# Performance work log

Hardware: AMD Instinct MI355X
Metric: run time of the kernel (lower is better)

The kernel has to match this reference:

```python
import jax, jax.numpy as jnp
import numpy as np

N_MEL = 80; ARNN = 1024; ADIM = 128; EMB = 512; PRE = 256; DRNN = 1024; NF = 32; KS = 31
B = 32; NCTX = 512; T = 500
PAD = (KS - 1) // 2


def setup_inputs() -> dict:
    key = jax.random.key(0)
    ks = jax.random.split(key, 20)
    g = lambda k, shape: jax.random.normal(k, shape, dtype=jnp.float32) * 0.02
    return {
        "memory": jax.random.normal(ks[0], (B, NCTX, EMB), dtype=jnp.float32),
        "decoder_inputs": jax.random.normal(ks[1], (B, N_MEL, T), dtype=jnp.float32),
        "mask": jnp.zeros((B, NCTX), dtype=bool),
        "prenet_w1": g(ks[2], (PRE, N_MEL)),
        "prenet_w2": g(ks[3], (PRE, PRE)),
        "arnn_wih": g(ks[4], (4 * ARNN, PRE + EMB)),
        "arnn_whh": g(ks[5], (4 * ARNN, ARNN)),
        "arnn_bih": jnp.zeros((4 * ARNN,), jnp.float32),
        "arnn_bhh": jnp.zeros((4 * ARNN,), jnp.float32),
        "q_w": g(ks[6], (ADIM, ARNN)),
        "m_w": g(ks[7], (ADIM, EMB)),
        "loc_conv_w": g(ks[8], (NF, 2, KS)),
        "loc_w": g(ks[9], (ADIM, NF)),
        "v_w": g(ks[10], (ADIM,)),
        "drnn_wih": g(ks[11], (4 * DRNN, ARNN + EMB)),
        "drnn_whh": g(ks[12], (4 * DRNN, DRNN)),
        "drnn_bih": jnp.zeros((4 * DRNN,), jnp.float32),
        "drnn_bhh": jnp.zeros((4 * DRNN,), jnp.float32),
        "proj_w": g(ks[13], (N_MEL, DRNN + EMB)),
        "proj_b": jnp.zeros((N_MEL,), jnp.float32),
        "gate_w": g(ks[14], (1, DRNN + EMB)),
        "gate_b": jnp.zeros((1,), jnp.float32),
    }


def _lstm_cell(x, h, c, wih, whh, bih, bhh):
    # PyTorch LSTMCell gate order: i, f, g, o
    z = x @ wih.T + h @ whh.T + bih + bhh
    i, f, g, o = jnp.split(z, 4, axis=-1)
    c2 = jax.nn.sigmoid(f) * c + jax.nn.sigmoid(i) * jnp.tanh(g)
    h2 = jax.nn.sigmoid(o) * jnp.tanh(c2)
    return h2, c2


def reference(memory, decoder_inputs, mask,
              prenet_w1, prenet_w2,
              arnn_wih, arnn_whh, arnn_bih, arnn_bhh,
              q_w, m_w, loc_conv_w, loc_w, v_w,
              drnn_wih, drnn_whh, drnn_bih, drnn_bhh,
              proj_w, proj_b, gate_w, gate_b):
    b, n_ctx, emb = memory.shape
    n_mel, t_out = decoder_inputs.shape[1], decoder_inputs.shape[2]

    # (time, batch, n_mel) with a leading zero go-frame; PreNet (eval: no dropout)
    x = jnp.transpose(decoder_inputs, (2, 0, 1))
    x = jnp.concatenate([jnp.zeros((1, b, n_mel), x.dtype), x], axis=0)
    h = jax.nn.relu(x @ prenet_w1.T)
    h = jax.nn.relu(h @ prenet_w2.T)  # (T+1, B, PRE)
    inputs = h[:-1]  # T decoder steps

    proc_mem = memory @ m_w.T  # (B, n_ctx, ADIM)

    def step(carry, xin):
        ah, ac, dh, dc, aw, awc, actx = carry
        cell_in = jnp.concatenate([xin, actx], axis=-1)
        ah, ac = _lstm_cell(cell_in, ah, ac, arnn_wih, arnn_whh, arnn_bih, arnn_bhh)
        # location-sensitive attention
        aw_cat = jnp.stack([aw, awc], axis=1)  # (B, 2, n_ctx)
        loc = jax.lax.conv_general_dilated(
            aw_cat, loc_conv_w, window_strides=(1,), padding=[(PAD, PAD)],
            dimension_numbers=("NCH", "OIH", "NCH"))  # (B, NF, n_ctx)
        loc = jnp.transpose(loc, (0, 2, 1)) @ loc_w.T  # (B, n_ctx, ADIM)
        q = (ah @ q_w.T)[:, None, :]  # (B, 1, ADIM)
        e = jnp.tanh(q + proc_mem + loc) @ v_w  # (B, n_ctx)
        e = jnp.where(mask, -1e9, e)
        aw = jax.nn.softmax(e, axis=-1)
        actx = jnp.einsum("bn,bne->be", aw, memory)
        awc = awc + aw
        din = jnp.concatenate([ah, actx], axis=-1)
        dh, dc = _lstm_cell(din, dh, dc, drnn_wih, drnn_whh, drnn_bih, drnn_bhh)
        dhc = jnp.concatenate([dh, actx], axis=-1)
        mel = dhc @ proj_w.T + proj_b  # (B, n_mel)
        gate = dhc @ gate_w.T + gate_b  # (B, 1)
        return (ah, ac, dh, dc, aw, awc, actx), (mel, gate[:, 0])

    z32 = lambda *s: jnp.zeros(s, memory.dtype)
    carry0 = (z32(b, ARNN), z32(b, ARNN), z32(b, DRNN), z32(b, DRNN),
              z32(b, n_ctx), z32(b, n_ctx), z32(b, emb))
    _, (mels, gates) = jax.lax.scan(step, carry0, inputs)
    mel_out = jnp.transpose(mels, (1, 2, 0))   # (B, n_mel, T)
    gate_out = jnp.transpose(gates, (1, 0))    # (B, T)
    return mel_out, gate_out
```

## Files before the change

kernel.cpp:

```cpp
#include <hip/hip_runtime.h>

#define NBLK 256
#define NTHR 512

constexpr int kNMel = 80, kArnn = 1024, kAdim = 128, kEmb = 512, kPre = 256;
constexpr int kNF = 32, kKS = 31, kB = 32, kNctx = 512, kT = 500, kPad = 15;

constexpr int KT_A = 56;
constexpr int KT_D = 80;
constexpr int KT_ALL = KT_A + KT_D;

constexpr int OFF_PREB   = 0;
constexpr int OFF_PROCMB = OFF_PREB + kT * kB * kPre / 2;
constexpr int OFF_QWTB   = OFF_PROCMB + kB * kNctx * kAdim / 2;
constexpr int OFF_LWT    = OFF_QWTB + kAdim * kArnn / 2;
constexpr int OFF_STATE  = OFF_LWT + kAdim * 33;
constexpr int OFF_AHB    = OFF_STATE;
constexpr int OFF_DHB    = OFF_AHB + 2 * kB * kArnn / 2;
constexpr int OFF_DH     = OFF_DHB + 2 * kB * kArnn / 2;
constexpr int OFF_AC     = OFF_DH + 2 * kB * kArnn;
constexpr int OFF_DC     = OFF_AC + kB * kArnn;
constexpr int OFF_ACTX   = OFF_DC + kB * kArnn;
constexpr int OFF_AW     = OFF_ACTX + kB * kEmb;
constexpr int OFF_AWC    = OFF_AW + kB * kNctx;
constexpr int OFF_PAW    = OFF_AWC + kB * kNctx;
constexpr int OFF_NUM    = OFF_PAW + kB * kNctx;
constexpr int OFF_DEN    = OFF_NUM + 2 * kB * kEmb;
constexpr int OFF_END    = OFF_DEN + 2 * kB;
constexpr int STATE_SZ   = OFF_END - OFF_STATE;
constexpr int OFF_BAR    = OFF_END;
constexpr int OFF_PAN    = (OFF_BAR + 16 + 3) & ~3;
constexpr int PAN_SZ     = NBLK * KT_ALL * 256;
constexpr int OFF_GMB    = OFF_PAN + PAN_SZ;
constexpr int GMB_SZ     = kB * kNctx * kEmb / 2;

typedef __attribute__((ext_vector_type(4))) float fvec4;
typedef __attribute__((ext_vector_type(8))) short bh8_t;
typedef unsigned long long u64;
typedef unsigned short ushortt;

union U64u { u64 u; float2 f2; ushortt s[4]; };

union SMem {
  struct { ushortt xs[8][2][2048]; } x1;
  struct { float zra[4][2][64][4]; float zrd[4][2][64][4];
           float hb[2][32][4]; } x2;
  struct { float ahb_s[kArnn]; float vw_s[kAdim]; float psum[512]; float q_s[kAdim];
           float aw_s[96]; float awc_s[96]; float cw[kNF * 2 * kKS];
           float loc_s[64 * 33]; float p_s[64]; float lwt[kAdim * 33];
           float dhc[kArnn + kEmb]; float pprj[126];
           ushortt pm[64 * kAdim]; } b;
  struct { float x8[8][80]; float h1[8][256]; } p;
  struct { float mem_s[4][512]; } m;
};

__device__ __forceinline__ float sigf(float x) { return 1.0f / (1.0f + __expf(-x)); }
__device__ __forceinline__ float tanhfast(float x) { return 1.0f - 2.0f / (__expf(2.0f * x) + 1.0f); }

__device__ __forceinline__ ushortt bf16rn(float f) {
  unsigned u = __float_as_uint(f);
  unsigned r = (u + 0x7FFFu + ((u >> 16) & 1u)) >> 16;
  return (ushortt)r;
}
__device__ __forceinline__ float bf2f(ushortt v) {
  return __uint_as_float((unsigned)v << 16);
}

__device__ __forceinline__ u64 ald64(const void* p) {
  return __hip_atomic_load((const u64*)p, __ATOMIC_RELAXED, __HIP_MEMORY_SCOPE_AGENT);
}
__device__ __forceinline__ float alf(const float* p) {
  return __hip_atomic_load(p, __ATOMIC_RELAXED, __HIP_MEMORY_SCOPE_AGENT);
}
__device__ __forceinline__ void asf(float* p, float v) {
  __hip_atomic_store(p, v, __ATOMIC_RELAXED, __HIP_MEMORY_SCOPE_AGENT);
}
__device__ __forceinline__ void as64(void* p, u64 v) {
  __hip_atomic_store((u64*)p, v, __ATOMIC_RELAXED, __HIP_MEMORY_SCOPE_AGENT);
}

__device__ __forceinline__ void gbar_full(unsigned* cnt, unsigned* gen, unsigned& genv) {
  __syncthreads();
  if (threadIdx.x == 0) {
    __threadfence();
    unsigned arrived = __hip_atomic_fetch_add(cnt, 1u, __ATOMIC_ACQ_REL, __HIP_MEMORY_SCOPE_AGENT) + 1u;
    if (arrived == (unsigned)NBLK) {
      __hip_atomic_store(cnt, 0u, __ATOMIC_RELAXED, __HIP_MEMORY_SCOPE_AGENT);
      __hip_atomic_fetch_add(gen, 1u, __ATOMIC_ACQ_REL, __HIP_MEMORY_SCOPE_AGENT);
    } else {
      while (__hip_atomic_load(gen, __ATOMIC_ACQUIRE, __HIP_MEMORY_SCOPE_AGENT) == genv) {
        __builtin_amdgcn_s_sleep(2);
      }
    }
    ++genv;
  }
  __syncthreads();
}

__device__ __forceinline__ void gbar_light(unsigned* cnt8, unsigned* root, unsigned* gen,
                                           unsigned& genv) {
  asm volatile("s_waitcnt vmcnt(0) lgkmcnt(0)" ::: "memory");
  __syncthreads();
  if (threadIdx.x == 0) {
    asm volatile("s_waitcnt vmcnt(0)" ::: "memory");
    int gi = blockIdx.x & 7;
    unsigned a = __hip_atomic_fetch_add(&cnt8[gi], 1u, __ATOMIC_RELAXED, __HIP_MEMORY_SCOPE_AGENT);
    if (a == 31u) {
      unsigned r = __hip_atomic_fetch_add(root, 1u, __ATOMIC_RELAXED, __HIP_MEMORY_SCOPE_AGENT);
      if (r == 7u) {
        #pragma unroll
        for (int i = 0; i < 8; ++i)
          __hip_atomic_store(&cnt8[i], 0u, __ATOMIC_RELAXED, __HIP_MEMORY_SCOPE_AGENT);
        __hip_atomic_store(root, 0u, __ATOMIC_RELAXED, __HIP_MEMORY_SCOPE_AGENT);
        asm volatile("s_waitcnt vmcnt(0)" ::: "memory");
        __hip_atomic_fetch_add(gen, 1u, __ATOMIC_RELAXED, __HIP_MEMORY_SCOPE_AGENT);
      }
    }
    while (__hip_atomic_load(gen, __ATOMIC_RELAXED, __HIP_MEMORY_SCOPE_AGENT) == genv) {
      __builtin_amdgcn_s_sleep(1);
    }
    ++genv;
  }
  __syncthreads();
}

template<int LS, int W>
__device__ __forceinline__ void lstm_wave(
    const ushortt* __restrict__ s0, const ushortt* __restrict__ s2,
    const float* __restrict__ numq, const float* __restrict__ invden,
    const short* __restrict__ pan,
    int l, ushortt* xstg, fvec4& z0, fvec4& z1)
{
  constexpr int NC  = LS ? 10 : 7;
  constexpr int CB  = LS ? W * 640 : W * 448;
  constexpr int KT0 = LS ? W * 20 : W * 14;
  constexpr int BD0 = LS ? 1024 : 256;
  constexpr int BD1 = LS ? 1536 : 768;
  const int u8 = l & 15, rj = l >> 4;
  const int m = l & 15, kg = l >> 4;

  u64 L0[8], L1[8];
  bh8_t f00, f01, f10, f11;

  auto load = [&](int c, u64* L, bh8_t& f0, bh8_t& f1) {
    const int c0 = CB + c * 64;
    if (c0 >= BD0 && c0 < BD1) {
      const float* base = numq + (c0 - BD0) + u8 * 4;
      #pragma unroll
      for (int j = 0; j < 8; ++j) {
        int row = 4 * j + rj;
        const float* fp = base + (size_t)row * kEmb;
        U64u a, b2; a.u = ald64(fp); b2.u = ald64(fp + 2);
        float s = invden[row];
        U64u pk;
        pk.s[0] = bf16rn(a.f2.x * s);  pk.s[1] = bf16rn(a.f2.y * s);
        pk.s[2] = bf16rn(b2.f2.x * s); pk.s[3] = bf16rn(b2.f2.y * s);
        L[j] = pk.u;
      }
    } else {
      const ushortt* bsrc; int stride; bool coh;
      if (c0 < BD0) { bsrc = s0 + c0;       stride = (LS ? 1024 : 256); coh = (LS == 1); }
      else          { bsrc = s2 + c0 - BD1; stride = 1024;              coh = true; }
      #pragma unroll
      for (int j = 0; j < 8; ++j) {
        const ushortt* ap = bsrc + (size_t)(4 * j + rj) * stride + u8 * 4;
        L[j] = coh ? ald64(ap) : *reinterpret_cast<const u64*>(ap);
      }
    }
    f0 = *reinterpret_cast<const bh8_t*>(pan + (size_t)(KT0 + c * 2) * 512 + l * 8);
    f1 = *reinterpret_cast<const bh8_t*>(pan + (size_t)(KT0 + c * 2 + 1) * 512 + l * 8);
  };
  auto stash = [&](int buf, u64* L) {
    #pragma unroll
    for (int j = 0; j < 8; ++j) {
      int row = 4 * j + rj;
      int sw = u8 ^ ((row & 7) << 1);
      *reinterpret_cast<u64*>(xstg + buf * 2048 + row * 64 + sw * 4) = L[j];
    }
  };
  auto consume = [&](int buf, bh8_t f0, bh8_t f1) {
    #pragma unroll
    for (int kt = 0; kt < 2; ++kt) {
      int sw = (2 * (kt * 4 + kg)) ^ ((m & 7) << 1);
      bh8_t a0 = *reinterpret_cast<const bh8_t*>(xstg + buf * 2048 + m * 64 + sw * 4);
      bh8_t a1 = *reinterpret_cast<const bh8_t*>(xstg + buf * 2048 + (16 + m) * 64 + sw * 4);
      bh8_t f = kt ? f1 : f0;
      z0 = __builtin_amdgcn_mfma_f32_16x16x32_bf16(a0, f, z0, 0, 0, 0);
      z1 = __builtin_amdgcn_mfma_f32_16x16x32_bf16(a1, f, z1, 0, 0, 0);
    }
  };

  load(0, L0, f00, f01);
  #pragma unroll
  for (int c = 0; c < NC; c += 2) {
    stash(0, L0);
    if (c + 1 < NC) load(c + 1, L1, f10, f11);
    consume(0, f00, f01);
    if (c + 1 < NC) {
      stash(1, L1);
      if (c + 2 < NC) load(c + 2, L0, f00, f01);
      consume(1, f10, f11);
    }
  }
}

extern "C" __global__ void __launch_bounds__(NTHR, 1)
decoder_kernel(const float* __restrict__ gmem, const float* __restrict__ dec,
               const unsigned char* __restrict__ mask,
               const float* __restrict__ pw1, const float* __restrict__ pw2,
               const float* __restrict__ awih, const float* __restrict__ awhh,
               const float* __restrict__ abih, const float* __restrict__ abhh,
               const float* __restrict__ qw, const float* __restrict__ mw,
               const float* __restrict__ cvw, const float* __restrict__ locw,
               const float* __restrict__ vw,
               const float* __restrict__ dwih, const float* __restrict__ dwhh,
               const float* __restrict__ dbih, const float* __restrict__ dbhh,
               const float* __restrict__ pjw, const float* __restrict__ pjb,
               const float* __restrict__ gw, const float* __restrict__ gb,
               float* __restrict__ out, float* __restrict__ ws, int useg)
{
  __shared__ SMem sm;
  __shared__ float s_invden[32];
  const int bk = blockIdx.x, tid = threadIdx.x;
  unsigned genv_f = 0, genv_l = 0;
  unsigned* bar = reinterpret_cast<unsigned*>(ws + OFF_BAR);
  unsigned* cnt8 = bar;
  unsigned* root = bar + 8;
  unsigned* genL = bar + 9;
  unsigned* cntF = bar + 10;
  unsigned* genF = bar + 11;

  ushortt* PREBu = reinterpret_cast<ushortt*>(ws + OFF_PREB);
  ushortt* PROCMBu = reinterpret_cast<ushortt*>(ws + OFF_PROCMB);
  ushortt* QWTBu = reinterpret_cast<ushortt*>(ws + OFF_QWTB);
  float* LWT = ws + OFF_LWT;
  ushortt* AHBu = reinterpret_cast<ushortt*>(ws + OFF_AHB);
  ushortt* DHBu = reinterpret_cast<ushortt*>(ws + OFF_DHB);
  float* DH = ws + OFF_DH;
  float* AC = ws + OFF_AC;
  float* DC = ws + OFF_DC;
  float* ACTX = ws + OFF_ACTX;
  float* AWp = ws + OFF_AW;
  float* AWC = ws + OFF_AWC;
  float* PAW = ws + OFF_PAW;
  float* NUM = ws + OFF_NUM;
  float* DEN = ws + OFF_DEN;
  short* PANS = reinterpret_cast<short*>(ws + OFF_PAN);
  ushortt* GMB = reinterpret_cast<ushortt*>(ws + OFF_GMB);

  for (int i = bk * NTHR + tid; i < STATE_SZ; i += NBLK * NTHR) (ws + OFF_STATE)[i] = 0.f;
  for (int i = bk * NTHR + tid; i < kAdim * kArnn; i += NBLK * NTHR)
    QWTBu[i] = bf16rn(qw[i]);
  for (int i = bk * NTHR + tid; i < kAdim * kNF; i += NBLK * NTHR) {
    int d = i >> 5, f = i & 31;
    LWT[d * 33 + f] = locw[i];
  }
  gbar_full(cntF, genF, genv_f);

  if (bk == 0 && tid < 2 * kB) asf(&DEN[tid], 1.0f);
  for (int it = 0; it < 16; ++it) {
    int task0 = bk * 64 + it * 4;
    for (int i = tid; i < 2048; i += NTHR) {
      int pr = i >> 9, h = i & 511;
      sm.m.mem_s[pr][h] = gmem[(size_t)(task0 + pr) * kEmb + h];
    }
    __syncthreads();
    {
      int pr = tid >> 7, d = tid & 127;
      const float* mwr = mw + d * kEmb;
      float acc = 0.f;
      for (int h = 0; h < kEmb; ++h) acc = fmaf(sm.m.mem_s[pr][h], mwr[h], acc);
      PROCMBu[(size_t)(task0 + pr) * kAdim + d] = bf16rn(acc);
    }
    if (useg) {
      for (int i = tid; i < 2048; i += NTHR) {
        int pr = i >> 9, h = i & 511;
        GMB[(size_t)(task0 + pr) * kEmb + h] = bf16rn(sm.m.mem_s[pr][h]);
      }
    }
    __syncthreads();
  }
  for (int g = bk; g < 2000; g += NBLK) {
    int t_idx = g >> 2;
    int b0 = (g & 3) * 8;
    if (t_idx == 0) {
      for (int i = tid; i < 8 * kPre; i += NTHR)
        PREBu[(size_t)(b0 + (i >> 8)) * kPre + (i & 255)] = 0;
      continue;
    }
    for (int i = tid; i < 640; i += NTHR) {
      int bb = i / 80, m2 = i % 80;
      sm.p.x8[bb][m2] = dec[((size_t)(b0 + bb) * kNMel + m2) * kT + (t_idx - 1)];
    }
    __syncthreads();
    {
      int u = tid & 255, rep = tid >> 8;
      float acc[4] = {0.f, 0.f, 0.f, 0.f};
      for (int m2 = 0; m2 < 80; ++m2) {
        float w = pw1[u * kNMel + m2];
        #pragma unroll
        for (int r = 0; r < 4; ++r) acc[r] = fmaf(w, sm.p.x8[rep * 4 + r][m2], acc[r]);
      }
      #pragma unroll
      for (int r = 0; r < 4; ++r) sm.p.h1[rep * 4 + r][u] = fmaxf(acc[r], 0.f);
    }
    __syncthreads();
    {
      int u = tid & 255, rep = tid >> 8;
      float acc[4] = {0.f, 0.f, 0.f, 0.f};
      for (int k = 0; k < kPre; ++k) {
        float w = pw2[u * kPre + k];
        #pragma unroll
        for (int r = 0; r < 4; ++r) acc[r] = fmaf(w, sm.p.h1[rep * 4 + r][k], acc[r]);
      }
      #pragma unroll
      for (int r = 0; r < 4; ++r)
        PREBu[((size_t)t_idx * kB + b0 + rep * 4 + r) * kPre + u] = bf16rn(fmaxf(acc[r], 0.f));
    }
    __syncthreads();
  }
  {
    const int UNITS = NBLK * KT_ALL * 64;
    for (int u = bk * NTHR + tid; u < UNITS; u += NBLK * NTHR) {
      int bkk = u / (KT_ALL * 64);
      int rem = u - bkk * (KT_ALL * 64);
      int kta = rem >> 6, l = rem & 63;
      int lstm = (kta >= KT_A);
      int kt = lstm ? kta - KT_A : kta;
      int n = l & 15, kg = l >> 4;
      int r = (n >> 2) * 1024 + bkk * 4 + (n & 3);
      bh8_t v;
      #pragma unroll
      for (int j = 0; j < 8; ++j) {
        int k = kt * 32 + kg * 8 + j;
        float wv;
        if (!lstm) wv = (k < 768) ? awih[(size_t)r * 768 + k] : awhh[(size_t)r * 1024 + (k - 768)];
        else       wv = (k < 1536) ? dwih[(size_t)r * 1536 + k] : dwhh[(size_t)r * 1024 + (k - 1536)];
        v[j] = (short)bf16rn(wv);
      }
      *reinterpret_cast<bh8_t*>(PANS + (size_t)u * 8) = v;
    }
  }
  gbar_full(cntF, genF, genv_f);

  for (int t = 0; t <= kT; ++t) {
    const int p = t & 1, q = p ^ 1;
    float* nump = NUM + p * kB * kEmb;
    const float* numq = NUM + q * kB * kEmb;

    if (tid < kB) s_invden[tid] = 1.0f / alf(DEN + q * kB + tid);
    __syncthreads();
    if (t > 0 && tid < 64) {
      int idx = bk * 64 + tid;
      int b2 = idx >> 9;
      float invd = s_invden[b2];
      float av = PAW[idx] * invd;
      asf(&AWp[idx], av);
      asf(&AWC[idx], alf(&AWC[idx]) + av);
      asf(&ACTX[idx], alf(&numq[idx]) * invd);
    }
    if (t < kT) {
      if (tid < 64) asf(&nump[bk * 64 + tid], 0.f);
      if (bk == 0 && tid < kB) asf(DEN + p * kB + tid, 0.f);
    }
    {
      const int w8 = tid >> 6, l = tid & 63;
      fvec4 z0 = {0.f, 0.f, 0.f, 0.f}, z1 = z0;
      const ushortt* AHBq_ = AHBu + q * kB * kArnn;
      const ushortt* DHBp_ = DHBu + p * kB * kArnn;
      const ushortt* preb_t = PREBu + (size_t)t * kB * kPre;
      ushortt* xst = &sm.x1.xs[w8][0][0];
      const short* panb = PANS + (size_t)bk * (KT_ALL * 512);
      const short* pand = panb + KT_A * 512;
      if (w8 < 4) {
        if (t < kT) {
          switch (w8) {
            case 0: lstm_wave<0,0>(preb_t, AHBq_, numq, s_invden, panb, l, xst, z0, z1); break;
            case 1: lstm_wave<0,1>(preb_t, AHBq_, numq, s_invden, panb, l, xst, z0, z1); break;
            case 2: lstm_wave<0,2>(preb_t, AHBq_, numq, s_invden, panb, l, xst, z0, z1); break;
            default: lstm_wave<0,3>(preb_t, AHBq_, numq, s_invden, panb, l, xst, z0, z1); break;
          }
        }
      } else {
        if (t > 0) {
          switch (w8) {
            case 4: lstm_wave<1,0>(AHBq_, DHBp_, numq, s_invden, pand, l, xst, z0, z1); break;
            case 5: lstm_wave<1,1>(AHBq_, DHBp_, numq, s_invden, pand, l, xst, z0, z1); break;
            case 6: lstm_wave<1,2>(AHBq_, DHBp_, numq, s_invden, pand, l, xst, z0, z1); break;
            default: lstm_wave<1,3>(AHBq_, DHBp_, numq, s_invden, pand, l, xst, z0, z1); break;
          }
        }
      }
      __syncthreads();
      if (w8 < 4) {
        *reinterpret_cast<fvec4*>(&sm.x2.zra[w8][0][l][0]) = z0;
        *reinterpret_cast<fvec4*>(&sm.x2.zra[w8][1][l][0]) = z1;
      } else {
        *reinterpret_cast<fvec4*>(&sm.x2.zrd[w8 - 4][0][l][0]) = z0;
        *reinterpret_cast<fvec4*>(&sm.x2.zrd[w8 - 4][1][l][0]) = z1;
      }
    }
    __syncthreads();
    if (tid < 256) {
      const int ls = tid >> 7, uu = (tid >> 5) & 3, b = tid & 31;
      const bool go = (ls == 0) ? (t < kT) : (t > 0);
      if (go) {
        const int mt = b >> 4, mm = b & 15;
        const int lane_base = (mm >> 2) * 16, rr = mm & 3;
        float zg[4];
        #pragma unroll
        for (int g = 0; g < 4; ++g) {
          int ln = lane_base + g * 4 + uu;
          float s;
          if (ls == 0)
            s = sm.x2.zra[0][mt][ln][rr] + sm.x2.zra[1][mt][ln][rr]
              + sm.x2.zra[2][mt][ln][rr] + sm.x2.zra[3][mt][ln][rr];
          else
            s = sm.x2.zrd[0][mt][ln][rr] + sm.x2.zrd[1][mt][ln][rr]
              + sm.x2.zrd[2][mt][ln][rr] + sm.x2.zrd[3][mt][ln][rr];
          int rg = g * 1024 + bk * 4 + uu;
          s += (ls ? dbih[rg] + dbhh[rg] : abih[rg] + abhh[rg]);
          zg[g] = s;
        }
        float* cst = ls ? DC : AC;
        const int idx = b * kArnn + bk * 4 + uu;
        float c = sigf(zg[1]) * cst[idx] + sigf(zg[0]) * tanhfast(zg[2]);
        cst[idx] = c;
        float h = sigf(zg[3]) * tanhfast(c);
        if (ls) asf(&DH[q * kB * kArnn + idx], h);
        sm.x2.hb[ls][b][uu] = h;
      }
    }
    __syncthreads();
    if (tid < 64) {
      int ls = tid >> 5, b = tid & 31;
      bool go2 = ls ? (t > 0) : (t < kT);
      if (go2) {
        U64u pk;
        #pragma unroll
        for (int j = 0; j < 4; ++j) pk.s[j] = bf16rn(sm.x2.hb[ls][b][j]);
        ushortt* dst = (ls ? (DHBu + q * kB * kArnn) : (AHBu + p * kB * kArnn)) + b * kArnn + bk * 4;
        as64(dst, pk.u);
      }
    }
    gbar_light(cnt8, root, genL, genv_l);

    if (t < kT) {
      const int b = bk >> 3, sub = bk & 7, j0 = sub * 64;
      const int pbase = (sub == 0) ? 0 : 21 + (sub - 1) * 20;
      const int pcnt = (sub == 0) ? 21 : 20;
      const ushortt* AHBp_ = AHBu + p * kB * kArnn;
      if (tid < 256) {
        U64u v; v.u = ald64(AHBp_ + b * kArnn + tid * 4);
        #pragma unroll
        for (int j = 0; j < 4; ++j) sm.b.ahb_s[tid * 4 + j] = bf2f(v.s[j]);
      }
      for (int i = tid; i < 94; i += NTHR) {
        int jj = j0 - kPad + i;
        bool ok = (jj >= 0 && jj < kNctx);
        sm.b.aw_s[i] = ok ? alf(&AWp[b * kNctx + jj]) : 0.f;
        sm.b.awc_s[i] = ok ? alf(&AWC[b * kNctx + jj]) : 0.f;
      }
      for (int i = tid; i < kNF * 2 * kKS; i += NTHR) sm.b.cw[i] = cvw[i];
      for (int i = tid; i < kAdim * 33; i += NTHR) sm.b.lwt[i] = LWT[i];
      for (int i = tid; i < kAdim; i += NTHR) sm.b.vw_s[i] = vw[i];
      {
        const fvec4* src = reinterpret_cast<const fvec4*>(PROCMBu + (size_t)(b * kNctx + j0) * kAdim);
        fvec4* dst = reinterpret_cast<fvec4*>(sm.b.pm);
        for (int i = tid; i < 1024; i += NTHR) dst[i] = src[i];
      }
      if (sub < 4 && t > 0) {
        for (int i = tid; i < kArnn + kEmb; i += NTHR)
          sm.b.dhc[i] = (i < kArnn) ? alf(&DH[q * kB * kArnn + b * kArnn + i])
                                    : alf(&ACTX[b * kEmb + (i - kArnn)]);
      }
      __syncthreads();
      {
        int d = tid & 127, qr = tid >> 7;
        const ushortt* wq = QWTBu + (size_t)d * kArnn + qr * 256;
        const float* ahs = sm.b.ahb_s + qr * 256;
        float acc = 0.f;
        #pragma unroll 4
        for (int h8 = 0; h8 < 32; ++h8) {
          U64u a, c2;
          a.u = *reinterpret_cast<const u64*>(wq + h8 * 8);
          c2.u = *reinterpret_cast<const u64*>(wq + h8 * 8 + 4);
          #pragma unroll
          for (int j = 0; j < 4; ++j) acc = fmaf(bf2f(a.s[j]), ahs[h8 * 8 + j], acc);
          #pragma unroll
          for (int j = 0; j < 4; ++j) acc = fmaf(bf2f(c2.s[j]), ahs[h8 * 8 + 4 + j], acc);
        }
        sm.b.psum[tid] = acc;
      }
      __syncthreads();
      if (tid < kAdim)
        sm.b.q_s[tid] = sm.b.psum[tid] + sm.b.psum[128 + tid]
                      + sm.b.psum[256 + tid] + sm.b.psum[384 + tid];
      {
        int j = tid >> 3, f0 = (tid & 7) * 4;
        #pragma unroll
        for (int fi = 0; fi < 4; ++fi) {
          int f = f0 + fi;
          const float* w0 = &sm.b.cw[f * 62];
          float s = 0.f;
          for (int k = 0; k < kKS; ++k)
            s = fmaf(sm.b.aw_s[j + k], w0[k], fmaf(sm.b.awc_s[j + k], w0[31 + k], s));
          sm.b.loc_s[j * 33 + f] = s;
        }
      }
      if (sub < 4 && t > 0 && tid < pcnt * 6) {
        int ol = tid / 6, kc = tid % 6, og = pbase + ol;
        const float* row = (og < kNMel) ? pjw + (size_t)og * (kArnn + kEmb) : gw;
        const float* x = sm.b.dhc + kc * 256;
        const float* r2 = row + kc * 256;
        float acc = 0.f;
        for (int k = 0; k < 256; ++k) acc = fmaf(r2[k], x[k], acc);
        sm.b.pprj[tid] = acc;
      }
      __syncthreads();
      {
        int j = tid >> 3, grp = tid & 7, jj = j0 + j;
        float pe = 0.f;
        #pragma unroll 4
        for (int dd = 0; dd < 16; ++dd) {
          int d = grp + 8 * dd;
          float l2 = 0.f;
          const float* ls2 = &sm.b.loc_s[j * 33];
          const float* lw2 = &sm.b.lwt[d * 33];
          #pragma unroll 8
          for (int f = 0; f < kNF; ++f) l2 = fmaf(ls2[f], lw2[f], l2);
          float x = sm.b.q_s[d] + bf2f(sm.b.pm[j * kAdim + d]) + l2;
          pe = fmaf(sm.b.vw_s[d], tanhfast(x), pe);
        }
        pe += __shfl_xor(pe, 1);
        pe += __shfl_xor(pe, 2);
        pe += __shfl_xor(pe, 4);
        if (grp == 0) {
          float pv = mask[b * kNctx + jj] ? 0.f : __expf(pe);
          sm.b.p_s[j] = pv;
          PAW[b * kNctx + jj] = pv;
        }
      }
      if (sub < 4 && t > 0 && tid < pcnt) {
        int og = pbase + tid;
        float val = (og < kNMel) ? pjb[og] : gb[0];
        #pragma unroll
        for (int kc = 0; kc < 6; ++kc) val += sm.b.pprj[tid * 6 + kc];
        if (og < kNMel) out[((size_t)b * kNMel + og) * kT + (t - 1)] = val;
        else out[(size_t)kB * kNMel * kT + b * kT + (t - 1)] = val;
      }
      __syncthreads();
      if (tid < 64) {
        float v = sm.b.p_s[tid];
        #pragma unroll
        for (int o = 1; o < 64; o <<= 1) v += __shfl_xor(v, o);
        if (tid == 0) atomicAdd(DEN + p * kB + b, v);
      }
      if (useg) {
        const ushortt* memb = GMB + (size_t)(b * kNctx + j0) * kEmb + tid;
        float a0 = 0.f, a1 = 0.f, a2 = 0.f, a3 = 0.f;
        #pragma unroll 4
        for (int jj2 = 0; jj2 < 64; jj2 += 4) {
          a0 = fmaf(sm.b.p_s[jj2],     bf2f(memb[(size_t)jj2 * kEmb]), a0);
          a1 = fmaf(sm.b.p_s[jj2 + 1], bf2f(memb[(size_t)(jj2 + 1) * kEmb]), a1);
          a2 = fmaf(sm.b.p_s[jj2 + 2], bf2f(memb[(size_t)(jj2 + 2) * kEmb]), a2);
          a3 = fmaf(sm.b.p_s[jj2 + 3], bf2f(memb[(size_t)(jj2 + 3) * kEmb]), a3);
        }
        atomicAdd(&nump[b * kEmb + tid], (a0 + a1) + (a2 + a3));
      } else {
        const float* memb = gmem + (size_t)(b * kNctx + j0) * kEmb + tid;
        float a0 = 0.f, a1 = 0.f;
        #pragma unroll 8
        for (int jj2 = 0; jj2 < 64; jj2 += 2) {
          a0 = fmaf(sm.b.p_s[jj2], memb[(size_t)jj2 * kEmb], a0);
          a1 = fmaf(sm.b.p_s[jj2 + 1], memb[(size_t)(jj2 + 1) * kEmb], a1);
        }
        atomicAdd(&nump[b * kEmb + tid], a0 + a1);
      }
      gbar_light(cnt8, root, genL, genv_l);
    }
  }

  if (bk < kB) {
    const int b = bk;
    for (int i = tid; i < kArnn + kEmb; i += NTHR)
      sm.b.dhc[i] = (i < kArnn) ? alf(&DH[1 * kB * kArnn + b * kArnn + i])
                                : alf(&ACTX[b * kEmb + (i - kArnn)]);
    __syncthreads();
    if (tid < 486) {
      int ol = tid / 6, kc = tid % 6;
      const float* row = (ol < kNMel) ? pjw + (size_t)ol * (kArnn + kEmb) : gw;
      const float* x = sm.b.dhc + kc * 256;
      const float* r2 = row + kc * 256;
      float acc = 0.f;
      for (int k = 0; k < 256; ++k) acc = fmaf(r2[k], x[k], acc);
      sm.b.psum[tid] = acc;
    }
    __syncthreads();
    if (tid < 81) {
      float val = (tid < kNMel) ? pjb[tid] : gb[0];
      #pragma unroll
      for (int kc = 0; kc < 6; ++kc) val += sm.b.psum[tid * 6 + kc];
      if (tid < kNMel) out[((size_t)b * kNMel + tid) * kT + (kT - 1)] = val;
      else out[(size_t)kB * kNMel * kT + b * kT + (kT - 1)] = val;
    }
  }
}

extern "C" void kernel_launch(void* const* d_in, const int* in_sizes, int n_in,
                              void* d_out, int out_size, void* d_ws, size_t ws_size,
                              hipStream_t stream) {
  const float* gmem = (const float*)d_in[0];
  const float* dec = (const float*)d_in[1];
  const unsigned char* mask = (const unsigned char*)d_in[2];
  const float* pw1 = (const float*)d_in[3];
  const float* pw2 = (const float*)d_in[4];
  const float* awih = (const float*)d_in[5];
  const float* awhh = (const float*)d_in[6];
  const float* abih = (const float*)d_in[7];
  const float* abhh = (const float*)d_in[8];
  const float* qw = (const float*)d_in[9];
  const float* mw = (const float*)d_in[10];
  const float* cvw = (const float*)d_in[11];
  const float* locw = (const float*)d_in[12];
  const float* vw = (const float*)d_in[13];
  const float* dwih = (const float*)d_in[14];
  const float* dwhh = (const float*)d_in[15];
  const float* dbih = (const float*)d_in[16];
  const float* dbhh = (const float*)d_in[17];
  const float* pjw = (const float*)d_in[18];
  const float* pjb = (const float*)d_in[19];
  const float* gw = (const float*)d_in[20];
  const float* gb = (const float*)d_in[21];
  float* out = (float*)d_out;
  float* ws = (float*)d_ws;

  int useg = (ws_size >= (size_t)(OFF_GMB + GMB_SZ) * sizeof(float)) ? 1 : 0;

  hipMemsetAsync((char*)d_ws + (size_t)OFF_BAR * sizeof(float), 0, 64, stream);
  hipLaunchKernelGGL(decoder_kernel, dim3(NBLK), dim3(NTHR), 0, stream,
                     gmem, dec, mask, pw1, pw2, awih, awhh, abih, abhh, qw, mw,
                     cvw, locw, vw, dwih, dwhh, dbih, dbhh, pjw, pjb, gw, gb,
                     out, ws, useg);
}
```

Measured before the change: 43.25 ms.

## Replace atomic-counter grid barrier with per-block flag barrier and master wave

Replaces the hierarchical atomic fetch-add grid barrier with a flag-based barrier. Each block writes a monotonically increasing epoch to its own 128-byte-padded slot, and one wave of block 0 polls all 256 slots in parallel. Once every slot has arrived, that wave releases eight padded wake flags, one per group of blocks. The aim is to cut contended atomic RMW traffic and serialized counter resets on the barrier that runs twice per timestep. The cost is a larger barrier region and a centralized polling block whose own arrival path becomes the critical path.

```diff
diff --git a/kernel.cpp b/kernel.cpp
--- a/kernel.cpp
+++ b/kernel.cpp
@@ -29,7 +29,8 @@
 constexpr int OFF_END    = OFF_DEN + 2 * kB;
 constexpr int STATE_SZ   = OFF_END - OFF_STATE;
 constexpr int OFF_BAR    = OFF_END;
-constexpr int OFF_PAN    = (OFF_BAR + 16 + 3) & ~3;
+constexpr int BAR_LINES  = 266;
+constexpr int OFF_PAN    = OFF_BAR + BAR_LINES * 32;
 constexpr int PAN_SZ     = NBLK * KT_ALL * 256;
 constexpr int OFF_GMB    = OFF_PAN + PAN_SZ;
 constexpr int GMB_SZ     = kB * kNctx * kEmb / 2;
@@ -78,6 +79,12 @@
 __device__ __forceinline__ void as64(void* p, u64 v) {
   __hip_atomic_store((u64*)p, v, __ATOMIC_RELAXED, __HIP_MEMORY_SCOPE_AGENT);
 }
+__device__ __forceinline__ unsigned alu(const unsigned* p) {
+  return __hip_atomic_load(p, __ATOMIC_RELAXED, __HIP_MEMORY_SCOPE_AGENT);
+}
+__device__ __forceinline__ void asu(unsigned* p, unsigned v) {
+  __hip_atomic_store(p, v, __ATOMIC_RELAXED, __HIP_MEMORY_SCOPE_AGENT);
+}
 
 __device__ __forceinline__ void gbar_full(unsigned* cnt, unsigned* gen, unsigned& genv) {
   __syncthreads();
@@ -97,29 +104,34 @@
   __syncthreads();
 }
 
-__device__ __forceinline__ void gbar_light(unsigned* cnt8, unsigned* root, unsigned* gen,
-                                           unsigned& genv) {
+__device__ __forceinline__ void gbar_light(unsigned* bar, unsigned target, int bk, int tid) {
   asm volatile("s_waitcnt vmcnt(0) lgkmcnt(0)" ::: "memory");
   __syncthreads();
-  if (threadIdx.x == 0) {
-    asm volatile("s_waitcnt vmcnt(0)" ::: "memory");
-    int gi = blockIdx.x & 7;
-    unsigned a = __hip_atomic_fetch_add(&cnt8[gi], 1u, __ATOMIC_RELAXED, __HIP_MEMORY_SCOPE_AGENT);
-    if (a == 31u) {
-      unsigned r = __hip_atomic_fetch_add(root, 1u, __ATOMIC_RELAXED, __HIP_MEMORY_SCOPE_AGENT);
-      if (r == 7u) {
-        #pragma unroll
-        for (int i = 0; i < 8; ++i)
-          __hip_atomic_store(&cnt8[i], 0u, __ATOMIC_RELAXED, __HIP_MEMORY_SCOPE_AGENT);
-        __hip_atomic_store(root, 0u, __ATOMIC_RELAXED, __HIP_MEMORY_SCOPE_AGENT);
+  if (bk == 0) {
+    if (tid < 64) {
+      if (tid == 0) {
         asm volatile("s_waitcnt vmcnt(0)" ::: "memory");
-        __hip_atomic_fetch_add(gen, 1u, __ATOMIC_RELAXED, __HIP_MEMORY_SCOPE_AGENT);
-      }
-    }
-    while (__hip_atomic_load(gen, __ATOMIC_RELAXED, __HIP_MEMORY_SCOPE_AGENT) == genv) {
-      __builtin_amdgcn_s_sleep(1);
-    }
-    ++genv;
+      }
+      unsigned i1 = (unsigned)tid * 4 + 1, i2 = i1 + 1, i3 = i1 + 2;
+      unsigned i0 = (unsigned)tid * 4;
+      for (;;) {
+        bool ok = true;
+        if (i0 != 0) ok = ok && (alu(&bar[i0 * 32]) >= target);
+        ok = ok && (alu(&bar[i1 * 32]) >= target);
+        ok = ok && (alu(&bar[i2 * 32]) >= target);
+        ok = ok && (alu(&bar[i3 * 32]) >= target);
+        if (__all(ok)) break;
+        __builtin_amdgcn_s_sleep(1);
+      }
+      if (tid < 8) asu(&bar[(256 + tid) * 32], target);
+    }
+  } else {
+    if (tid == 0) {
+      asm volatile("s_waitcnt vmcnt(0)" ::: "memory");
+      asu(&bar[bk * 32], target);
+      unsigned* wk = &bar[(256 + (bk & 7)) * 32];
+      while (alu(wk) < target) __builtin_amdgcn_s_sleep(1);
+    }
   }
   __syncthreads();
 }
@@ -222,13 +234,10 @@
   __shared__ SMem sm;
   __shared__ float s_invden[32];
   const int bk = blockIdx.x, tid = threadIdx.x;
-  unsigned genv_f = 0, genv_l = 0;
+  unsigned genv_f = 0, bcnt = 0;
   unsigned* bar = reinterpret_cast<unsigned*>(ws + OFF_BAR);
-  unsigned* cnt8 = bar;
-  unsigned* root = bar + 8;
-  unsigned* genL = bar + 9;
-  unsigned* cntF = bar + 10;
-  unsigned* genF = bar + 11;
+  unsigned* cntF = &bar[264 * 32];
+  unsigned* genF = &bar[265 * 32];
 
   ushortt* PREBu = reinterpret_cast<ushortt*>(ws + OFF_PREB);
   ushortt* PROCMBu = reinterpret_cast<ushortt*>(ws + OFF_PROCMB);
@@ -443,7 +452,7 @@
         as64(dst, pk.u);
       }
     }
-    gbar_light(cnt8, root, genL, genv_l);
+    gbar_light(bar, ++bcnt, bk, tid);
 
     if (t < kT) {
       const int b = bk >> 3, sub = bk & 7, j0 = sub * 64;
@@ -577,7 +586,7 @@
         }
         atomicAdd(&nump[b * kEmb + tid], a0 + a1);
       }
-      gbar_light(cnt8, root, genL, genv_l);
+      gbar_light(bar, ++bcnt, bk, tid);
     }
   }
 
@@ -637,7 +646,8 @@
 
   int useg = (ws_size >= (size_t)(OFF_GMB + GMB_SZ) * sizeof(float)) ? 1 : 0;
 
-  hipMemsetAsync((char*)d_ws + (size_t)OFF_BAR * sizeof(float), 0, 64, stream);
+  hipMemsetAsync((char*)d_ws + (size_t)OFF_BAR * sizeof(float), 0,
+                 (size_t)BAR_LINES * 128, stream);
   hipLaunchKernelGGL(decoder_kernel, dim3(NBLK), dim3(NTHR), 0, stream,
                      gmem, dec, mask, pw1, pw2, awih, awhh, abih, abhh, qw, mw,
                      cvw, locw, vw, dwih, dwhh, dbih, dbhh, pjw, pjb, gw, gb,
```

Result: faster. 38.91 ms (-10.0%).
